# Performance work log

Hardware: AMD Instinct MI355X
Metric: run time of the kernel (lower is better)

The kernel has to match this reference:

```python
import jax, jax.numpy as jnp
import numpy as np
from jax import lax

TOP_K = 4
N_GROUP = 4
TOPK_GROUP = 2
ROUTED_SCALING = 2.5
NORM_TOPK = True


def relu2(v):
    r = jax.nn.relu(v)
    return r * r


def setup_inputs() -> dict:
    key = jax.random.key(0)
    ks = jax.random.split(key, 7)
    B, S, H, E, I, IS = 2, 2048, 1024, 16, 512, 2048
    x = jax.random.normal(ks[0], (B, S, H), dtype=jnp.float32)
    router_w = jax.random.normal(ks[1], (E, H), dtype=jnp.float32) * 0.02
    bias = jnp.zeros((E,), dtype=jnp.float32)
    w_up = jax.random.normal(ks[2], (E, I, H), dtype=jnp.float32) * 0.02
    w_down = jax.random.normal(ks[3], (E, H, I), dtype=jnp.float32) * 0.02
    ws_up = jax.random.normal(ks[4], (IS, H), dtype=jnp.float32) * 0.02
    ws_down = jax.random.normal(ks[5], (H, IS), dtype=jnp.float32) * 0.02
    return {"x": x, "router_w": router_w, "bias": bias, "w_up": w_up,
            "w_down": w_down, "ws_up": ws_up, "ws_down": ws_down,
            "attn_metadata": 0}


def _route(xf, router_w, bias):
    # xf: [T, H] float32
    T = xf.shape[0]
    E = router_w.shape[0]
    logits = xf @ router_w.T                      # [T, E]
    scores = jax.nn.sigmoid(logits)
    sfc = scores + bias[None, :]                  # scores_for_choice
    # group scores: sum of top-2 within each group
    g = sfc.reshape(T, N_GROUP, E // N_GROUP)
    group_scores = lax.top_k(g, 2)[0].sum(-1)     # [T, G]
    _, gidx = lax.top_k(group_scores, TOPK_GROUP)
    gmask = jax.nn.one_hot(gidx, N_GROUP, dtype=sfc.dtype).sum(1)  # [T, G]
    smask = jnp.repeat(gmask, E // N_GROUP, axis=1)                # [T, E]
    masked = jnp.where(smask > 0, sfc, 0.0)
    _, tidx = lax.top_k(masked, TOP_K)            # [T, K]
    tw = jnp.take_along_axis(scores, tidx, axis=1)
    if NORM_TOPK:
        tw = tw / (tw.sum(-1, keepdims=True) + 1e-20)
    tw = tw * ROUTED_SCALING
    return tidx, tw


def reference(x, router_w, bias, w_up, w_down, ws_up, ws_down, attn_metadata):
    B, S, H = x.shape
    E = w_up.shape[0]
    xf = x.reshape(-1, H).astype(jnp.float32)     # [T, H]
    tidx, tw = _route(xf, router_w, bias)
    # combine weights per (token, expert): scatter-add topk weights
    T = xf.shape[0]
    comb = jnp.zeros((T, E), dtype=tw.dtype).at[jnp.arange(T)[:, None], tidx].add(tw)
    # routed experts (dense grouped form; zero combine weight == not routed)
    up = jnp.einsum('th,eih->tei', xf, w_up)      # [T, E, I]
    h = relu2(up) * comb[:, :, None]
    routed = jnp.einsum('tei,ehi->th', h, w_down) # [T, H]
    routed = routed.reshape(B, S, H).astype(x.dtype)
    # shared expert on residual
    shared = relu2(jnp.einsum('bsh,ih->bsi', x, ws_up))
    shared = jnp.einsum('bsi,hi->bsh', shared, ws_down)
    return routed + shared
```

## Files before the change

### kernel.cpp

```cpp
#include <hip/hip_runtime.h>
#include <stdint.h>

#define T_TOK 4096
#define H_DIM 1024
#define E_NUM 16
#define I_DIM 512
#define IS_DIM 2048
#define TOPK 4
#define NGRP 4
#define GSZ 4
#define MAXMT 32
#define NCHUNK 64

typedef unsigned short u16;
typedef __attribute__((ext_vector_type(8))) short short8;
typedef __attribute__((ext_vector_type(4))) float f32x4;

__device__ __forceinline__ void gload16(const void* g, void* l) {
  __builtin_amdgcn_global_load_lds(
      (const __attribute__((address_space(1))) void*)g,
      (__attribute__((address_space(3))) void*)l, 16, 0, 0);
}

__device__ __forceinline__ u16 f2bf(float f) {
  union { float f; uint32_t u; } v; v.f = f;
  uint32_t u = v.u;
  uint32_t r = (u + 0x7fffu + ((u >> 16) & 1u)) >> 16;
  return (u16)r;
}

__device__ __forceinline__ float bf2f(u16 h) {
  union { uint32_t u; float f; } v; v.u = ((uint32_t)h) << 16;
  return v.f;
}

__global__ __launch_bounds__(256) void cvt_bf16_kernel(const float* __restrict__ in,
                                                       u16* __restrict__ out, int n4) {
  int i = blockIdx.x * 256 + threadIdx.x;
  if (i >= n4) return;
  float4 v = reinterpret_cast<const float4*>(in)[i];
  ushort4 o;
  o.x = f2bf(v.x); o.y = f2bf(v.y); o.z = f2bf(v.z); o.w = f2bf(v.w);
  reinterpret_cast<ushort4*>(out)[i] = o;
}

__global__ __launch_bounds__(256) void route_kernel(
    const float* __restrict__ x, const float* __restrict__ rw,
    const float* __restrict__ bias, int* __restrict__ tidx_out,
    float* __restrict__ tw_out) {
  const int wave = threadIdx.x >> 6;
  const int lane = threadIdx.x & 63;
  const int t = blockIdx.x * 4 + wave;

  const float4* xr = reinterpret_cast<const float4*>(x + (size_t)t * H_DIM);
  const float4* rw4 = reinterpret_cast<const float4*>(rw);
  float4 xv[4];
#pragma unroll
  for (int j = 0; j < 4; ++j) xv[j] = xr[lane + j * 64];

  double acc[E_NUM];
#pragma unroll
  for (int e = 0; e < E_NUM; ++e) {
    double a = 0.0;
#pragma unroll
    for (int j = 0; j < 4; ++j) {
      float4 w = rw4[e * 256 + lane + j * 64];
      a += (double)xv[j].x * (double)w.x;
      a += (double)xv[j].y * (double)w.y;
      a += (double)xv[j].z * (double)w.z;
      a += (double)xv[j].w * (double)w.w;
    }
    acc[e] = a;
  }
#pragma unroll
  for (int e = 0; e < E_NUM; ++e) {
#pragma unroll
    for (int off = 32; off; off >>= 1) acc[e] += __shfl_xor(acc[e], off);
  }
  if (lane == 0) {
    float scores[E_NUM], sfc[E_NUM];
#pragma unroll
    for (int e = 0; e < E_NUM; ++e) {
      scores[e] = 1.0f / (1.0f + expf((float)(-acc[e])));
      sfc[e] = scores[e] + bias[e];
    }
    float gs[NGRP];
#pragma unroll
    for (int g = 0; g < NGRP; ++g) {
      float m1 = -1e30f, m2 = -1e30f;
#pragma unroll
      for (int j = 0; j < GSZ; ++j) {
        float v = sfc[g * GSZ + j];
        if (v > m1) { m2 = m1; m1 = v; } else if (v > m2) { m2 = v; }
      }
      gs[g] = m1 + m2;
    }
    int g1 = 0;
    for (int g = 1; g < NGRP; ++g) if (gs[g] > gs[g1]) g1 = g;
    int g2 = -1;
    for (int g = 0; g < NGRP; ++g) {
      if (g == g1) continue;
      if (g2 < 0 || gs[g] > gs[g2]) g2 = g;
    }
    float masked[E_NUM];
#pragma unroll
    for (int e = 0; e < E_NUM; ++e) {
      int g = e / GSZ;
      masked[e] = (g == g1 || g == g2) ? sfc[e] : 0.0f;
    }
    int tidx[TOPK]; float tw[TOPK];
#pragma unroll
    for (int k = 0; k < TOPK; ++k) {
      int best = 0; float bv = masked[0];
      for (int e = 1; e < E_NUM; ++e)
        if (masked[e] > bv) { bv = masked[e]; best = e; }
      tidx[k] = best; tw[k] = scores[best]; masked[best] = -1e30f;
    }
    float s = tw[0] + tw[1] + tw[2] + tw[3] + 1e-20f;
#pragma unroll
    for (int k = 0; k < TOPK; ++k) {
      tidx_out[t * TOPK + k] = tidx[k];
      tw_out[t * TOPK + k] = tw[k] / s * 2.5f;
    }
  }
}

__global__ __launch_bounds__(256) void hist_kernel(const int* __restrict__ tidx,
                                                   int* __restrict__ partial) {
  const int c = blockIdx.x;
  const int tid = threadIdx.x;
  const int lane = tid & 63;
  const int w = tid >> 6;
  __shared__ int h[4][E_NUM];
  const int e = tidx[c * 256 + tid];
#pragma unroll
  for (int ee = 0; ee < E_NUM; ++ee) {
    unsigned long long b = __ballot(e == ee);
    if (lane == 0) h[w][ee] = __popcll(b);
  }
  __syncthreads();
  if (tid < E_NUM)
    partial[c * E_NUM + tid] = h[0][tid] + h[1][tid] + h[2][tid] + h[3][tid];
}

__global__ __launch_bounds__(256) void prefix2_kernel(
    const int* __restrict__ partial, int* __restrict__ chunk_base,
    int* __restrict__ counts, int* __restrict__ offsets) {
  __shared__ int tot[E_NUM];
  __shared__ int offs[E_NUM];
  const int tid = threadIdx.x;
  if (tid < E_NUM) {
    int run = 0;
    for (int c = 0; c < NCHUNK; ++c) {
      chunk_base[c * E_NUM + tid] = run;
      run += partial[c * E_NUM + tid];
    }
    tot[tid] = run;
    counts[tid] = run;
  }
  __syncthreads();
  if (tid == 0) {
    int s = 0;
    for (int e = 0; e < E_NUM; ++e) { offs[e] = s; offsets[e] = s; s += tot[e]; }
    offsets[E_NUM] = s;
  }
  __syncthreads();
  for (int i = tid; i < NCHUNK * E_NUM; i += 256)
    chunk_base[i] += offs[i & 15];
}

__global__ __launch_bounds__(256) void scatter2_kernel(
    const int* __restrict__ tidx, const float* __restrict__ tw,
    const int* __restrict__ chunk_base,
    int* __restrict__ tok_g, float* __restrict__ w_g, int* __restrict__ pos_map) {
  const int c = blockIdx.x;
  const int tid = threadIdx.x;
  const int lane = tid & 63;
  const int w = tid >> 6;
  __shared__ int h[4][E_NUM];
  const int i = c * 256 + tid;
  const int e = tidx[i];
  int pre = 0;
#pragma unroll
  for (int ee = 0; ee < E_NUM; ++ee) {
    unsigned long long b = __ballot(e == ee);
    if (lane == 0) h[w][ee] = __popcll(b);
    if (ee == e) pre = __popcll(b & ((1ull << lane) - 1ull));
  }
  __syncthreads();
  int rank = pre;
  for (int ww = 0; ww < w; ++ww) rank += h[ww][e];
  const int pos = chunk_base[c * E_NUM + e] + rank;
  tok_g[pos] = i >> 2;
  w_g[pos] = tw[i];
  pos_map[i] = pos;
}

template <int EPI>
__global__ __launch_bounds__(512, 4) void gemm_bt(
    const u16* __restrict__ Abase, const u16* __restrict__ Bbase,
    float* __restrict__ Cf, u16* __restrict__ Cb,
    int M, int N, int K,
    const int* __restrict__ counts, const int* __restrict__ offsets,
    const int* __restrict__ tok_g, const float* __restrict__ w_g,
    const int* __restrict__ pos_map, const u16* __restrict__ Rd) {
  __shared__ __align__(16) u16 As[2][128 * 64];
  __shared__ __align__(16) u16 Bs[2][128 * 64];

  const int NT = N >> 7;
  int mt, nt, cnt = M, obase = 0;
  const u16* A = Abase;
  const u16* B = Bbase;

  if constexpr (EPI <= 1) {
    mt = blockIdx.x / NT;
    nt = blockIdx.x - mt * NT;
  } else {
    const int per_e = MAXMT * NT;
    int e = blockIdx.x / per_e;
    int r = blockIdx.x - e * per_e;
    mt = r / NT;
    nt = r - mt * NT;
    cnt = counts[e];
    if (mt * 128 >= cnt) return;
    obase = offsets[e];
    if constexpr (EPI == 2) {
      B = Bbase + (size_t)e * (I_DIM * H_DIM);
    } else {
      A = Abase + (size_t)obase * I_DIM;
      B = Bbase + (size_t)e * (H_DIM * I_DIM);
    }
  }

  const int tid = threadIdx.x;
  const int srow = tid >> 3;
  const int slot = tid & 7;
  const u16* gA[2];
  const u16* gB[2];
#pragma unroll
  for (int p = 0; p < 2; ++p) {
    int rloc = p * 64 + srow;
    int ks = ((slot ^ (rloc & 7)) << 3);
    int am = mt * 128 + rloc;
    if constexpr (EPI == 2) {
      int tk = tok_g[obase + ((am < cnt) ? am : 0)];
      gA[p] = Abase + (size_t)tk * H_DIM + ks;
    } else if constexpr (EPI == 3) {
      gA[p] = A + (size_t)((am < cnt) ? am : 0) * K + ks;
    } else {
      gA[p] = A + (size_t)am * K + ks;
    }
    gB[p] = B + (size_t)(nt * 128 + rloc) * K + ks;
  }

  const int wave = tid >> 6;
  const int lane = tid & 63;
  const int wr = wave >> 2;
  const int wc = wave & 3;
  const int frow = lane & 15;
  const int l4 = lane >> 4;

  int a_off[4][2], b_off[2][2];
#pragma unroll
  for (int m = 0; m < 4; ++m) {
    int row = wr * 64 + m * 16 + frow;
#pragma unroll
    for (int kk = 0; kk < 2; ++kk)
      a_off[m][kk] = (row << 6) + ((((kk << 2) + l4) ^ (row & 7)) << 3);
  }
#pragma unroll
  for (int n = 0; n < 2; ++n) {
    int row = wc * 32 + n * 16 + frow;
#pragma unroll
    for (int kk = 0; kk < 2; ++kk)
      b_off[n][kk] = (row << 6) + ((((kk << 2) + l4) ^ (row & 7)) << 3);
  }

  f32x4 acc[4][2];
#pragma unroll
  for (int m = 0; m < 4; ++m)
#pragma unroll
    for (int n = 0; n < 2; ++n) acc[m][n] = (f32x4)0.0f;

  const int dst = tid << 3;
  auto stage = [&](int k0, int c) {
#pragma unroll
    for (int p = 0; p < 2; ++p)
      gload16(gA[p] + k0, &As[c][(p << 12) + dst]);
#pragma unroll
    for (int p = 0; p < 2; ++p)
      gload16(gB[p] + k0, &Bs[c][(p << 12) + dst]);
  };

  const int KT = K >> 6;
  stage(0, 0);
  int cur = 0;
  for (int kt = 0; kt < KT; ++kt) {
    __syncthreads();
    if (kt + 1 < KT) stage((kt + 1) << 6, cur ^ 1);
#pragma unroll
    for (int kk = 0; kk < 2; ++kk) {
      short8 a[4], b[2];
#pragma unroll
      for (int m = 0; m < 4; ++m)
        a[m] = *reinterpret_cast<const short8*>(&As[cur][a_off[m][kk]]);
#pragma unroll
      for (int n = 0; n < 2; ++n)
        b[n] = *reinterpret_cast<const short8*>(&Bs[cur][b_off[n][kk]]);
#pragma unroll
      for (int m = 0; m < 4; ++m)
#pragma unroll
        for (int n = 0; n < 2; ++n)
          acc[m][n] = __builtin_amdgcn_mfma_f32_16x16x32_bf16(a[m], b[n], acc[m][n], 0, 0, 0);
    }
    cur ^= 1;
  }

  const int rbase = l4 << 2;
  const int cbase = frow;
#pragma unroll
  for (int m = 0; m < 4; ++m) {
#pragma unroll
    for (int r = 0; r < 4; ++r) {
      int lr = wr * 64 + (m << 4) + rbase + r;
      int grow = mt * 128 + lr;
      if (EPI >= 2 && grow >= cnt) continue;
      float wv = 1.0f;
      if constexpr (EPI == 2) wv = w_g[obase + grow];
      const int* pm = nullptr;
      if constexpr (EPI == 1) pm = pos_map + grow * TOPK;
#pragma unroll
      for (int n = 0; n < 2; ++n) {
        int gc = nt * 128 + wc * 32 + (n << 4) + cbase;
        float v = acc[m][n][r];
        if constexpr (EPI == 0) {
          float tpos = fmaxf(v, 0.0f);
          Cb[(size_t)grow * N + gc] = f2bf(tpos * tpos);
        } else if constexpr (EPI == 1) {
          v += bf2f(Rd[(size_t)pm[0] * H_DIM + gc]);
          v += bf2f(Rd[(size_t)pm[1] * H_DIM + gc]);
          v += bf2f(Rd[(size_t)pm[2] * H_DIM + gc]);
          v += bf2f(Rd[(size_t)pm[3] * H_DIM + gc]);
          Cf[(size_t)grow * N + gc] = v;
        } else if constexpr (EPI == 2) {
          float tpos = fmaxf(v, 0.0f);
          Cb[(size_t)(obase + grow) * I_DIM + gc] = f2bf(tpos * tpos * wv);
        } else {
          Cb[(size_t)(obase + grow) * N + gc] = f2bf(v);
        }
      }
    }
  }
}

extern "C" void kernel_launch(void* const* d_in, const int* in_sizes, int n_in,
                              void* d_out, int out_size, void* d_ws, size_t ws_size,
                              hipStream_t stream) {
  const float* x = (const float*)d_in[0];
  const float* rw = (const float*)d_in[1];
  const float* bias = (const float*)d_in[2];
  const float* w_up = (const float*)d_in[3];
  const float* w_down = (const float*)d_in[4];
  const float* ws_up = (const float*)d_in[5];
  const float* ws_down = (const float*)d_in[6];
  float* out = (float*)d_out;

  uint8_t* wsb = (uint8_t*)d_ws;
  size_t off = 0;
  auto alloc = [&](size_t bytes) {
    void* p = wsb + off;
    off += (bytes + 255) & ~(size_t)255;
    return p;
  };
  u16* x_bf = (u16*)alloc((size_t)T_TOK * H_DIM * 2);
  u16* wsup_bf = (u16*)alloc((size_t)IS_DIM * H_DIM * 2);
  u16* wsdn_bf = (u16*)alloc((size_t)H_DIM * IS_DIM * 2);
  u16* wup_bf = (u16*)alloc((size_t)E_NUM * I_DIM * H_DIM * 2);
  u16* wdn_bf = (u16*)alloc((size_t)E_NUM * H_DIM * I_DIM * 2);
  u16* hs = (u16*)alloc((size_t)T_TOK * IS_DIM * 2);
  u16* hp = (u16*)alloc((size_t)(T_TOK * TOPK + 128) * I_DIM * 2);
  u16* hp_down = (u16*)alloc((size_t)(T_TOK * TOPK + 128) * H_DIM * 2);
  int* counts = (int*)alloc(64);
  int* offsets = (int*)alloc(128);
  int* tok_g = (int*)alloc((size_t)(T_TOK * TOPK) * 4);
  float* w_g = (float*)alloc((size_t)(T_TOK * TOPK) * 4);
  int* pos_map = (int*)alloc((size_t)(T_TOK * TOPK) * 4);
  int* tidx_buf = (int*)alloc((size_t)T_TOK * TOPK * 4);
  float* tw_buf = (float*)alloc((size_t)T_TOK * TOPK * 4);
  int* partial = (int*)alloc((size_t)NCHUNK * E_NUM * 4);
  int* chunk_base = (int*)alloc((size_t)NCHUNK * E_NUM * 4);

  int n4;
  n4 = T_TOK * H_DIM / 4;
  cvt_bf16_kernel<<<(n4 + 255) / 256, 256, 0, stream>>>(x, x_bf, n4);
  n4 = IS_DIM * H_DIM / 4;
  cvt_bf16_kernel<<<(n4 + 255) / 256, 256, 0, stream>>>(ws_up, wsup_bf, n4);
  n4 = H_DIM * IS_DIM / 4;
  cvt_bf16_kernel<<<(n4 + 255) / 256, 256, 0, stream>>>(ws_down, wsdn_bf, n4);
  n4 = E_NUM * I_DIM * H_DIM / 4;
  cvt_bf16_kernel<<<(n4 + 255) / 256, 256, 0, stream>>>(w_up, wup_bf, n4);
  n4 = E_NUM * H_DIM * I_DIM / 4;
  cvt_bf16_kernel<<<(n4 + 255) / 256, 256, 0, stream>>>(w_down, wdn_bf, n4);

  route_kernel<<<T_TOK / 4, 256, 0, stream>>>(x, rw, bias, tidx_buf, tw_buf);
  hist_kernel<<<NCHUNK, 256, 0, stream>>>(tidx_buf, partial);
  prefix2_kernel<<<1, 256, 0, stream>>>(partial, chunk_base, counts, offsets);
  scatter2_kernel<<<NCHUNK, 256, 0, stream>>>(tidx_buf, tw_buf, chunk_base,
                                              tok_g, w_g, pos_map);

  gemm_bt<0><<<(T_TOK / 128) * (IS_DIM / 128), 512, 0, stream>>>(
      x_bf, wsup_bf, nullptr, hs, T_TOK, IS_DIM, H_DIM,
      nullptr, nullptr, nullptr, nullptr, nullptr, nullptr);
  gemm_bt<2><<<E_NUM * MAXMT * (I_DIM / 128), 512, 0, stream>>>(
      x_bf, wup_bf, nullptr, hp, T_TOK, I_DIM, H_DIM,
      counts, offsets, tok_g, w_g, nullptr, nullptr);
  gemm_bt<3><<<E_NUM * MAXMT * (H_DIM / 128), 512, 0, stream>>>(
      hp, wdn_bf, nullptr, hp_down, T_TOK, H_DIM, I_DIM,
      counts, offsets, tok_g, w_g, nullptr, nullptr);
  gemm_bt<1><<<(T_TOK / 128) * (H_DIM / 128), 512, 0, stream>>>(
      hs, wsdn_bf, out, nullptr, T_TOK, H_DIM, IS_DIM,
      nullptr, nullptr, nullptr, nullptr, pos_map, hp_down);
}
```

Baseline: 208.1 us.

## Triple-buffer GEMM with 256 threads, BK=32, and fuse bf16 conversions

The GEMM now uses 256-thread blocks where each wave computes a 64x64 tile (4x4 MFMAs), with K-step 32 and a three-stage LDS ring. Explicit vmcnt waits let two tiles stay in flight. It also adds s_setprio around the MFMA block and a new swizzle for the 64-byte rows. The five separate fp32-to-bf16 conversion launches are merged into one kernel to cut launch overhead. The risk is higher register pressure from 16 accumulators per wave, and the wait counts are hand-tuned, so they are fragile.

```diff
diff --git a/kernel.cpp b/kernel.cpp
--- a/kernel.cpp
+++ b/kernel.cpp
@@ -12,6 +12,12 @@
 #define MAXMT 32
 #define NCHUNK 64
 
+#define S0 1048576
+#define S1 1572864
+#define S2 2097152
+#define S3 4194304
+#define S4 6291456
+
 typedef unsigned short u16;
 typedef __attribute__((ext_vector_type(8))) short short8;
 typedef __attribute__((ext_vector_type(4))) float f32x4;
@@ -34,14 +40,23 @@
   return v.f;
 }
 
-__global__ __launch_bounds__(256) void cvt_bf16_kernel(const float* __restrict__ in,
-                                                       u16* __restrict__ out, int n4) {
+__global__ __launch_bounds__(256) void cvt_all_kernel(
+    const float* __restrict__ x, const float* __restrict__ wsu,
+    const float* __restrict__ wsd, const float* __restrict__ wu,
+    const float* __restrict__ wd,
+    u16* __restrict__ xb, u16* __restrict__ wsub, u16* __restrict__ wsdb,
+    u16* __restrict__ wub, u16* __restrict__ wdb) {
   int i = blockIdx.x * 256 + threadIdx.x;
-  if (i >= n4) return;
-  float4 v = reinterpret_cast<const float4*>(in)[i];
+  const float4* src; ushort4* dst; int base;
+  if (i < S0)      { src = (const float4*)x;   dst = (ushort4*)xb;   base = 0;  }
+  else if (i < S1) { src = (const float4*)wsu; dst = (ushort4*)wsub; base = S0; }
+  else if (i < S2) { src = (const float4*)wsd; dst = (ushort4*)wsdb; base = S1; }
+  else if (i < S3) { src = (const float4*)wu;  dst = (ushort4*)wub;  base = S2; }
+  else             { src = (const float4*)wd;  dst = (ushort4*)wdb;  base = S3; }
+  float4 v = src[i - base];
   ushort4 o;
   o.x = f2bf(v.x); o.y = f2bf(v.y); o.z = f2bf(v.z); o.w = f2bf(v.w);
-  reinterpret_cast<ushort4*>(out)[i] = o;
+  dst[i - base] = o;
 }
 
 __global__ __launch_bounds__(256) void route_kernel(
@@ -197,15 +212,15 @@
 }
 
 template <int EPI>
-__global__ __launch_bounds__(512, 4) void gemm_bt(
+__global__ __launch_bounds__(256, 3) void gemm_bt(
     const u16* __restrict__ Abase, const u16* __restrict__ Bbase,
     float* __restrict__ Cf, u16* __restrict__ Cb,
     int M, int N, int K,
     const int* __restrict__ counts, const int* __restrict__ offsets,
     const int* __restrict__ tok_g, const float* __restrict__ w_g,
     const int* __restrict__ pos_map, const u16* __restrict__ Rd) {
-  __shared__ __align__(16) u16 As[2][128 * 64];
-  __shared__ __align__(16) u16 Bs[2][128 * 64];
+  __shared__ __align__(16) u16 As[3][128 * 32];
+  __shared__ __align__(16) u16 Bs[3][128 * 32];
 
   const int NT = N >> 7;
   int mt, nt, cnt = M, obase = 0;
@@ -233,14 +248,14 @@
   }
 
   const int tid = threadIdx.x;
-  const int srow = tid >> 3;
-  const int slot = tid & 7;
+  const int srow = tid >> 2;
+  const int sphys = tid & 3;
   const u16* gA[2];
   const u16* gB[2];
 #pragma unroll
   for (int p = 0; p < 2; ++p) {
     int rloc = p * 64 + srow;
-    int ks = ((slot ^ (rloc & 7)) << 3);
+    int ks = ((sphys ^ ((rloc >> 1) & 3)) << 3);
     int am = mt * 128 + rloc;
     if constexpr (EPI == 2) {
       int tk = tok_g[obase + ((am < cnt) ? am : 0)];
@@ -255,65 +270,70 @@
 
   const int wave = tid >> 6;
   const int lane = tid & 63;
-  const int wr = wave >> 2;
-  const int wc = wave & 3;
+  const int wr = wave >> 1;
+  const int wc = wave & 1;
   const int frow = lane & 15;
   const int l4 = lane >> 4;
 
-  int a_off[4][2], b_off[2][2];
+  int a_off[4], b_off[4];
 #pragma unroll
   for (int m = 0; m < 4; ++m) {
     int row = wr * 64 + m * 16 + frow;
-#pragma unroll
-    for (int kk = 0; kk < 2; ++kk)
-      a_off[m][kk] = (row << 6) + ((((kk << 2) + l4) ^ (row & 7)) << 3);
-  }
-#pragma unroll
-  for (int n = 0; n < 2; ++n) {
-    int row = wc * 32 + n * 16 + frow;
-#pragma unroll
-    for (int kk = 0; kk < 2; ++kk)
-      b_off[n][kk] = (row << 6) + ((((kk << 2) + l4) ^ (row & 7)) << 3);
-  }
-
-  f32x4 acc[4][2];
+    a_off[m] = (row << 5) + ((l4 ^ ((row >> 1) & 3)) << 3);
+  }
+#pragma unroll
+  for (int n = 0; n < 4; ++n) {
+    int row = wc * 64 + n * 16 + frow;
+    b_off[n] = (row << 5) + ((l4 ^ ((row >> 1) & 3)) << 3);
+  }
+
+  f32x4 acc[4][4];
 #pragma unroll
   for (int m = 0; m < 4; ++m)
 #pragma unroll
-    for (int n = 0; n < 2; ++n) acc[m][n] = (f32x4)0.0f;
+    for (int n = 0; n < 4; ++n) acc[m][n] = (f32x4)0.0f;
 
   const int dst = tid << 3;
   auto stage = [&](int k0, int c) {
 #pragma unroll
     for (int p = 0; p < 2; ++p)
-      gload16(gA[p] + k0, &As[c][(p << 12) + dst]);
+      gload16(gA[p] + k0, &As[c][(p << 11) + dst]);
 #pragma unroll
     for (int p = 0; p < 2; ++p)
-      gload16(gB[p] + k0, &Bs[c][(p << 12) + dst]);
+      gload16(gB[p] + k0, &Bs[c][(p << 11) + dst]);
   };
 
-  const int KT = K >> 6;
+  const int KT = K >> 5;
   stage(0, 0);
-  int cur = 0;
+  stage(32, 1);
+  int cb = 0, sb = 2;
   for (int kt = 0; kt < KT; ++kt) {
-    __syncthreads();
-    if (kt + 1 < KT) stage((kt + 1) << 6, cur ^ 1);
-#pragma unroll
-    for (int kk = 0; kk < 2; ++kk) {
-      short8 a[4], b[2];
-#pragma unroll
-      for (int m = 0; m < 4; ++m)
-        a[m] = *reinterpret_cast<const short8*>(&As[cur][a_off[m][kk]]);
-#pragma unroll
-      for (int n = 0; n < 2; ++n)
-        b[n] = *reinterpret_cast<const short8*>(&Bs[cur][b_off[n][kk]]);
-#pragma unroll
-      for (int m = 0; m < 4; ++m)
-#pragma unroll
-        for (int n = 0; n < 2; ++n)
-          acc[m][n] = __builtin_amdgcn_mfma_f32_16x16x32_bf16(a[m], b[n], acc[m][n], 0, 0, 0);
-    }
-    cur ^= 1;
+    if (kt < KT - 1) {
+      asm volatile("s_waitcnt vmcnt(4)" ::: "memory");
+    } else {
+      asm volatile("s_waitcnt vmcnt(0)" ::: "memory");
+    }
+    __builtin_amdgcn_s_barrier();
+    __builtin_amdgcn_sched_barrier(0);
+    if (kt + 2 < KT) stage((kt + 2) << 5, sb);
+    const u16* Ab = &As[cb][0];
+    const u16* Bb = &Bs[cb][0];
+    short8 a[4], b[4];
+#pragma unroll
+    for (int m = 0; m < 4; ++m)
+      a[m] = *reinterpret_cast<const short8*>(Ab + a_off[m]);
+#pragma unroll
+    for (int n = 0; n < 4; ++n)
+      b[n] = *reinterpret_cast<const short8*>(Bb + b_off[n]);
+    __builtin_amdgcn_s_setprio(1);
+#pragma unroll
+    for (int m = 0; m < 4; ++m)
+#pragma unroll
+      for (int n = 0; n < 4; ++n)
+        acc[m][n] = __builtin_amdgcn_mfma_f32_16x16x32_bf16(a[m], b[n], acc[m][n], 0, 0, 0);
+    __builtin_amdgcn_s_setprio(0);
+    cb = (cb == 2) ? 0 : cb + 1;
+    sb = (sb == 2) ? 0 : sb + 1;
   }
 
   const int rbase = l4 << 2;
@@ -330,8 +350,8 @@
       const int* pm = nullptr;
       if constexpr (EPI == 1) pm = pos_map + grow * TOPK;
 #pragma unroll
-      for (int n = 0; n < 2; ++n) {
-        int gc = nt * 128 + wc * 32 + (n << 4) + cbase;
+      for (int n = 0; n < 4; ++n) {
+        int gc = nt * 128 + wc * 64 + (n << 4) + cbase;
         float v = acc[m][n][r];
         if constexpr (EPI == 0) {
           float tpos = fmaxf(v, 0.0f);
@@ -390,17 +410,9 @@
   int* partial = (int*)alloc((size_t)NCHUNK * E_NUM * 4);
   int* chunk_base = (int*)alloc((size_t)NCHUNK * E_NUM * 4);
 
-  int n4;
-  n4 = T_TOK * H_DIM / 4;
-  cvt_bf16_kernel<<<(n4 + 255) / 256, 256, 0, stream>>>(x, x_bf, n4);
-  n4 = IS_DIM * H_DIM / 4;
-  cvt_bf16_kernel<<<(n4 + 255) / 256, 256, 0, stream>>>(ws_up, wsup_bf, n4);
-  n4 = H_DIM * IS_DIM / 4;
-  cvt_bf16_kernel<<<(n4 + 255) / 256, 256, 0, stream>>>(ws_down, wsdn_bf, n4);
-  n4 = E_NUM * I_DIM * H_DIM / 4;
-  cvt_bf16_kernel<<<(n4 + 255) / 256, 256, 0, stream>>>(w_up, wup_bf, n4);
-  n4 = E_NUM * H_DIM * I_DIM / 4;
-  cvt_bf16_kernel<<<(n4 + 255) / 256, 256, 0, stream>>>(w_down, wdn_bf, n4);
+  cvt_all_kernel<<<S4 / 256, 256, 0, stream>>>(
+      x, ws_up, ws_down, w_up, w_down,
+      x_bf, wsup_bf, wsdn_bf, wup_bf, wdn_bf);
 
   route_kernel<<<T_TOK / 4, 256, 0, stream>>>(x, rw, bias, tidx_buf, tw_buf);
   hist_kernel<<<NCHUNK, 256, 0, stream>>>(tidx_buf, partial);
@@ -408,16 +420,16 @@
   scatter2_kernel<<<NCHUNK, 256, 0, stream>>>(tidx_buf, tw_buf, chunk_base,
                                               tok_g, w_g, pos_map);
 
-  gemm_bt<0><<<(T_TOK / 128) * (IS_DIM / 128), 512, 0, stream>>>(
+  gemm_bt<0><<<(T_TOK / 128) * (IS_DIM / 128), 256, 0, stream>>>(
       x_bf, wsup_bf, nullptr, hs, T_TOK, IS_DIM, H_DIM,
       nullptr, nullptr, nullptr, nullptr, nullptr, nullptr);
-  gemm_bt<2><<<E_NUM * MAXMT * (I_DIM / 128), 512, 0, stream>>>(
+  gemm_bt<2><<<E_NUM * MAXMT * (I_DIM / 128), 256, 0, stream>>>(
       x_bf, wup_bf, nullptr, hp, T_TOK, I_DIM, H_DIM,
       counts, offsets, tok_g, w_g, nullptr, nullptr);
-  gemm_bt<3><<<E_NUM * MAXMT * (H_DIM / 128), 512, 0, stream>>>(
+  gemm_bt<3><<<E_NUM * MAXMT * (H_DIM / 128), 256, 0, stream>>>(
       hp, wdn_bf, nullptr, hp_down, T_TOK, H_DIM, I_DIM,
       counts, offsets, tok_g, w_g, nullptr, nullptr);
-  gemm_bt<1><<<(T_TOK / 128) * (H_DIM / 128), 512, 0, stream>>>(
+  gemm_bt<1><<<(T_TOK / 128) * (H_DIM / 128), 256, 0, stream>>>(
       hs, wsdn_bf, out, nullptr, T_TOK, H_DIM, IS_DIM,
       nullptr, nullptr, nullptr, nullptr, pos_map, hp_down);
 }
```

Result: no change. 206.9 us (-0.6%).
